# Performance work log

Hardware: AMD Instinct MI355X
Metric: run time of the kernel (lower is better)

The kernel has to match this reference:

```python
import jax, jax.numpy as jnp
import numpy as np
from jax import lax

SHIFT_SIZE = 5
PAD = SHIFT_SIZE // 2


def _chunk_shifts(C):
    # torch.chunk(x, 5, dim=1): chunk size = ceil(C/5); shift for chunk i is i - PAD
    csz = -(-C // SHIFT_SIZE)
    return jnp.arange(C) // csz - PAD  # (C,) in [-PAD, PAD]


def _shift_along_h(x, shifts):
    # x: (B,C,H,W). Equivalent of pad+chunk+roll(dim=2)+cat+narrow: per-channel
    # zero-filled shift along H (no wraparound since |shift| <= PAD).
    B, C, H, W = x.shape
    xp = jnp.pad(x, ((0, 0), (0, 0), (PAD, PAD), (0, 0)))
    c_idx = jnp.arange(C)[:, None]              # (C,1)
    h_idx = jnp.arange(H)[None, :] + PAD - shifts[:, None]  # (C,H)
    return xp[:, c_idx, h_idx, :]               # (B,C,H,W)


def _shift_along_w(x, shifts):
    return jnp.swapaxes(_shift_along_h(jnp.swapaxes(x, 2, 3), shifts), 2, 3)


def setup_inputs() -> dict:
    key = jax.random.key(0)
    ks = jax.random.split(key, 7)
    B, H, W, C, hidden = 8, 128, 128, 256, 256
    x = jax.random.normal(ks[0], (B, H * W, C), dtype=jnp.float32)
    w1 = jax.random.normal(ks[1], (hidden, C), dtype=jnp.float32) * 0.02
    b1 = jnp.zeros((hidden,), dtype=jnp.float32)
    fan_out = 3 * 3 * hidden // hidden  # groups = hidden
    dw_w = jax.random.normal(ks[2], (hidden, 1, 3, 3), dtype=jnp.float32) * np.sqrt(2.0 / fan_out)
    dw_b = jnp.zeros((hidden,), dtype=jnp.float32)
    w2 = jax.random.normal(ks[3], (C, hidden), dtype=jnp.float32) * 0.02
    b2 = jnp.zeros((C,), dtype=jnp.float32)
    return {"x": x, "H": H, "W": W, "w1": w1, "b1": b1,
            "dw_w": dw_w, "dw_b": dw_b, "w2": w2, "b2": b2}


def reference(x, H, W, w1, b1, dw_w, dw_b, w2, b2):
    B, N, C = x.shape
    shifts = _chunk_shifts(C)

    # --- shift along H, then fc1 ---
    xn = jnp.reshape(jnp.swapaxes(x, 1, 2), (B, C, H, W))
    x_s = _shift_along_h(xn, shifts)
    x_s = jnp.swapaxes(x_s.reshape(B, C, H * W), 1, 2)   # (B,N,C)
    h = x_s @ w1.T + b1                                  # (B,N,hidden)

    # --- depthwise 3x3 conv ---
    Ch = h.shape[-1]
    himg = jnp.reshape(jnp.swapaxes(h, 1, 2), (B, Ch, H, W))
    himg = lax.conv_general_dilated(
        himg, dw_w, window_strides=(1, 1), padding=((1, 1), (1, 1)),
        feature_group_count=Ch,
        dimension_numbers=("NCHW", "OIHW", "NCHW")) + dw_b[None, :, None, None]
    h = jnp.swapaxes(himg.reshape(B, Ch, H * W), 1, 2)

    h = jax.nn.gelu(h, approximate=False)

    # --- shift along W, then fc2 ---
    hn = jnp.reshape(jnp.swapaxes(h, 1, 2), (B, Ch, H, W))
    h_s = _shift_along_w(hn, _chunk_shifts(Ch))
    h_s = jnp.swapaxes(h_s.reshape(B, Ch, H * W), 1, 2)  # (B,N,hidden)
    out = h_s @ w2.T + b2                                # (B,N,C)
    return out
```

## Files before the change

### kernel.cpp

```cpp
#include <hip/hip_runtime.h>
#include <hip/hip_bf16.h>
#include <math.h>

#define Hc   128
#define Wc   128
#define Cc   256
#define Nc   (Hc * Wc)
#define Bn   8
#define Mtot (Bn * Nc)
#define CSZ  52
#define SPAD 2

typedef unsigned short ushort4v __attribute__((ext_vector_type(4)));
typedef unsigned short ushort8  __attribute__((ext_vector_type(8)));
typedef __bf16         bf16x8   __attribute__((ext_vector_type(8)));
typedef float          f32x4    __attribute__((ext_vector_type(4)));

__device__ __forceinline__ float bf2f(unsigned short u) {
    return __uint_as_float(((unsigned)u) << 16);
}
__device__ __forceinline__ unsigned short f2bf(float f) {
    unsigned u = __float_as_uint(f);
    return (unsigned short)((u + 0x7fffu + ((u >> 16) & 1u)) >> 16);
}
__device__ __forceinline__ unsigned pk2bf(float a, float b) {
    unsigned ua = __float_as_uint(a) + 0x8000u;
    unsigned ub = __float_as_uint(b) + 0x8000u;
    return __builtin_amdgcn_perm(ub, ua, 0x07060302);
}
__device__ __forceinline__ void async16(const void* g, void* l) {
    __builtin_amdgcn_global_load_lds(
        (const __attribute__((address_space(1))) unsigned*)g,
        (__attribute__((address_space(3))) unsigned*)l, 16, 0, 0);
}

__global__ __launch_bounds__(256)
void wprep_kernel(const float* __restrict__ w1, const float* __restrict__ w2,
                  const float* __restrict__ dw_w,
                  unsigned short* __restrict__ w1b, unsigned short* __restrict__ w2b,
                  float* __restrict__ dwT)
{
    const int g = blockIdx.x * 256 + threadIdx.x;
    {
        float4 a = *(const float4*)(w1 + (size_t)g * 4);
        ushort4v o = { f2bf(a.x), f2bf(a.y), f2bf(a.z), f2bf(a.w) };
        *(ushort4v*)(w1b + (size_t)g * 4) = o;
    }
    {
        float4 a = *(const float4*)(w2 + (size_t)g * 4);
        ushort4v o = { f2bf(a.x), f2bf(a.y), f2bf(a.z), f2bf(a.w) };
        *(ushort4v*)(w2b + (size_t)g * 4) = o;
    }
    if (g < 9 * Cc) dwT[(g % 9) * Cc + g / 9] = dw_w[g];
}

__global__ __launch_bounds__(256)
void shiftcvt_kernel(const float* __restrict__ x, unsigned short* __restrict__ xb)
{
    const int gid0 = blockIdx.x * 256 + threadIdx.x;
#pragma unroll
    for (int it = 0; it < 4; ++it) {
        const int gid = gid0 + it * (4096 * 256);
        const int row = gid >> 5;
        const int c   = (gid & 31) * 8;
        const int hh  = (row >> 7) & 127;
        const int s0  = c / CSZ - SPAD;
        const int s1  = (c + 4) / CSZ - SPAD;
        const int h0  = hh - s0, h1r = hh - s1;
        float4 v0 = make_float4(0.f, 0.f, 0.f, 0.f);
        float4 v1 = make_float4(0.f, 0.f, 0.f, 0.f);
        if (h0  >= 0 && h0  < Hc)
            v0 = *(const float4*)(x + ((size_t)row + (size_t)(h0 - hh) * Wc) * Cc + c);
        if (h1r >= 0 && h1r < Hc)
            v1 = *(const float4*)(x + ((size_t)row + (size_t)(h1r - hh) * Wc) * Cc + c + 4);
        uint4 o;
        o.x = pk2bf(v0.x, v0.y); o.y = pk2bf(v0.z, v0.w);
        o.z = pk2bf(v1.x, v1.y); o.w = pk2bf(v1.z, v1.w);
        *(uint4*)(xb + (size_t)row * Cc + c) = o;
    }
}

__global__ __launch_bounds__(256)
void fc1_mfma_kernel(const unsigned short* __restrict__ xb, const unsigned short* __restrict__ w1b,
                     const float* __restrict__ b1, unsigned short* __restrict__ h1)
{
    __shared__ __align__(16) unsigned char smem[34816];
    __bf16* As = (__bf16*)smem;
    __bf16* Bs = (__bf16*)(smem + 16384);
    unsigned short* Cs = (unsigned short*)smem;

    const int tid  = threadIdx.x;
    const int lane = tid & 63;
    const int wave = tid >> 6;
    const int wm = (wave >> 1) * 64, wn = (wave & 1) * 64;

    const int lid = ((blockIdx.x & 7) << 8) | (blockIdx.x >> 3);
    const int bx  = lid >> 1;
    const int j0  = (lid & 1) * 128;
    const size_t m0 = (size_t)bx * 128;
    const int idx0 = tid, idx1 = tid + 256;

    const size_t aro0 = (m0 + (idx0 >> 2)) * Cc + (idx0 & 3) * 8;
    const size_t aro1 = (m0 + (idx1 >> 2)) * Cc + (idx1 & 3) * 8;
    const size_t bro0 = (size_t)(j0 + (idx0 >> 2)) * Cc + (idx0 & 3) * 8;
    const size_t bro1 = (size_t)(j0 + (idx1 >> 2)) * Cc + (idx1 & 3) * 8;

    auto stage = [&](int buf, int t) {
        const int k0 = t * 32;
        __bf16* adst = As + buf * 4096;
        __bf16* bdst = Bs + buf * 4096;
        async16(xb  + aro0 + k0, adst + idx0 * 8);
        async16(xb  + aro1 + k0, adst + idx1 * 8);
        async16(w1b + bro0 + k0, bdst + idx0 * 8);
        async16(w1b + bro1 + k0, bdst + idx1 * 8);
    };

    f32x4 acc[4][4] = {};
    const int kq = (lane >> 4) * 8;
    const int rr = lane & 15;

    stage(0, 0);
    __syncthreads();

    int cur = 0;
    for (int t = 0; t < 8; ++t) {
        const int nxt = cur ^ 1;
        if (t < 7) stage(nxt, t + 1);
        bf16x8 a[4], b[4];
        const __bf16* ap = As + cur * 4096;
        const __bf16* bp = Bs + cur * 4096;
#pragma unroll
        for (int i = 0; i < 4; ++i) {
            a[i] = *(const bf16x8*)(ap + (wm + i * 16 + rr) * 32 + kq);
            b[i] = *(const bf16x8*)(bp + (wn + i * 16 + rr) * 32 + kq);
        }
#pragma unroll
        for (int i = 0; i < 4; ++i)
#pragma unroll
            for (int j = 0; j < 4; ++j)
                acc[i][j] = __builtin_amdgcn_mfma_f32_16x16x32_bf16(a[i], b[j], acc[i][j], 0, 0, 0);
        __syncthreads();
        cur = nxt;
    }

    const int cq = (lane >> 4) * 4;
    const int cc = lane & 15;
    float bv[4];
#pragma unroll
    for (int j = 0; j < 4; ++j) bv[j] = b1[j0 + wn + j * 16 + cc];
#pragma unroll
    for (int i = 0; i < 4; ++i)
#pragma unroll
        for (int j = 0; j < 4; ++j) {
            const int col = wn + j * 16 + cc;
#pragma unroll
            for (int rg = 0; rg < 4; ++rg)
                Cs[(wm + i * 16 + cq + rg) * 136 + col] = f2bf(acc[i][j][rg] + bv[j]);
        }
    __syncthreads();
    {
        const int row = tid >> 1, hf = tid & 1;
        const unsigned short* src = Cs + row * 136 + hf * 64;
        unsigned short* dst = h1 + (m0 + row) * Cc + j0 + hf * 64;
#pragma unroll
        for (int i = 0; i < 8; ++i)
            *(uint4*)(dst + i * 8) = *(const uint4*)(src + i * 8);
    }
}

__global__ __launch_bounds__(256)
void zero_borders_kernel(unsigned short* __restrict__ gsh)
{
    const int gid = blockIdx.x * 256 + threadIdx.x;
    const int cg  = gid & 31;
    const int rest = gid >> 5;
    const int wi = rest & 3;
    const int bh = rest >> 2;
    const int w  = (wi & 2) ? (wi + 124) : wi;
    uint4 z; z.x = z.y = z.z = z.w = 0u;
    *(uint4*)(gsh + ((size_t)bh * 128 + w) * Cc + cg * 8) = z;
}

__global__ __launch_bounds__(256)
void dwconv_gelu_scatter_kernel(const unsigned short* __restrict__ h1,
                                const float* __restrict__ dwT, const float* __restrict__ dw_b,
                                unsigned short* __restrict__ gsh)
{
    const int t   = threadIdx.x;
    const int cg  = t & 31;
    const int wq  = t >> 5;
    const int c0  = cg * 8;
    const int bh  = blockIdx.x >> 2;
    const int qtr = blockIdx.x & 3;
    const int bb  = bh >> 7, hh = bh & 127;
    const size_t rowb = (size_t)bb * Nc + (size_t)hh * Wc;
    const int wbase = qtr * 32 + wq * 4 - 1;

    float acc[4][8];
    {
        float4 a0 = *(const float4*)(dw_b + c0);
        float4 a1 = *(const float4*)(dw_b + c0 + 4);
#pragma unroll
        for (int i = 0; i < 4; ++i) {
            acc[i][0] = a0.x; acc[i][1] = a0.y; acc[i][2] = a0.z; acc[i][3] = a0.w;
            acc[i][4] = a1.x; acc[i][5] = a1.y; acc[i][6] = a1.z; acc[i][7] = a1.w;
        }
    }

#pragma unroll
    for (int dy = -1; dy <= 1; ++dy) {
        const int y = hh + dy;
        if (y < 0 || y >= Hc) continue;
        const unsigned short* rp = h1 + ((size_t)bb * Nc + (size_t)y * Wc) * Cc + c0;
        float in[6][8];
#pragma unroll
        for (int dx = 0; dx < 6; ++dx) {
            const int w = wbase + dx;
            ushort8 raw = {0, 0, 0, 0, 0, 0, 0, 0};
            if (w >= 0 && w < Wc) raw = *(const ushort8*)(rp + (size_t)w * Cc);
#pragma unroll
            for (int c = 0; c < 8; ++c) in[dx][c] = bf2f(raw[c]);
        }
        const float* wrow = dwT + (dy + 1) * 3 * Cc + c0;
        float wr[3][8];
#pragma unroll
        for (int tx = 0; tx < 3; ++tx) {
            float4 wa = *(const float4*)(wrow + tx * Cc);
            float4 wb = *(const float4*)(wrow + tx * Cc + 4);
            wr[tx][0] = wa.x; wr[tx][1] = wa.y; wr[tx][2] = wa.z; wr[tx][3] = wa.w;
            wr[tx][4] = wb.x; wr[tx][5] = wb.y; wr[tx][6] = wb.z; wr[tx][7] = wb.w;
        }
#pragma unroll
        for (int i = 0; i < 4; ++i)
#pragma unroll
            for (int tx = 0; tx < 3; ++tx)
#pragma unroll
                for (int c = 0; c < 8; ++c)
                    acc[i][c] += in[i + tx][c] * wr[tx][c];
    }

    const int s0 = c0 / CSZ - SPAD;
    const int s1 = (c0 + 4) / CSZ - SPAD;
#pragma unroll
    for (int i = 0; i < 4; ++i) {
        float g[8];
#pragma unroll
        for (int c = 0; c < 8; ++c) {
            const float v = acc[i][c];
            const float u = v * v;
            const float a = __builtin_fmaf(0.0713548162f, u, 1.5957691216f);
            const float e = __expf(v * a);
            g[c] = v * e * __builtin_amdgcn_rcpf(e + 1.0f);
        }
        uint2 lo, hi;
        lo.x = pk2bf(g[0], g[1]); lo.y = pk2bf(g[2], g[3]);
        hi.x = pk2bf(g[4], g[5]); hi.y = pk2bf(g[6], g[7]);
        const int wo = wbase + 1 + i;
        const int w0 = wo + s0, w1 = wo + s1;
        if ((unsigned)w0 < (unsigned)Wc) *(uint2*)(gsh + (rowb + w0) * Cc + c0)     = lo;
        if ((unsigned)w1 < (unsigned)Wc) *(uint2*)(gsh + (rowb + w1) * Cc + c0 + 4) = hi;
    }
}

__global__ __launch_bounds__(256)
void fc2_mfma_kernel(const unsigned short* __restrict__ A, const unsigned short* __restrict__ w2b,
                     const float* __restrict__ b2, float* __restrict__ out)
{
    __shared__ __align__(16) unsigned char smem[32768];
    __bf16* As = (__bf16*)smem;
    __bf16* Bs = (__bf16*)(smem + 16384);

    const int tid  = threadIdx.x;
    const int lane = tid & 63;
    const int wave = tid >> 6;
    const int wm = (wave >> 1) * 64, wn = (wave & 1) * 64;

    const int lid = ((blockIdx.x & 7) << 8) | (blockIdx.x >> 3);
    const size_t m0 = (size_t)(lid >> 1) * 128;
    const int j0 = (lid & 1) * 128;
    const int idx0 = tid, idx1 = tid + 256;

    const size_t aro0 = (m0 + (idx0 >> 2)) * Cc + (idx0 & 3) * 8;
    const size_t aro1 = (m0 + (idx1 >> 2)) * Cc + (idx1 & 3) * 8;
    const size_t bro0 = (size_t)(j0 + (idx0 >> 2)) * Cc + (idx0 & 3) * 8;
    const size_t bro1 = (size_t)(j0 + (idx1 >> 2)) * Cc + (idx1 & 3) * 8;

    auto stage = [&](int buf, int t) {
        const int k0 = t * 32;
        __bf16* adst = As + buf * 4096;
        __bf16* bdst = Bs + buf * 4096;
        async16(A   + aro0 + k0, adst + idx0 * 8);
        async16(A   + aro1 + k0, adst + idx1 * 8);
        async16(w2b + bro0 + k0, bdst + idx0 * 8);
        async16(w2b + bro1 + k0, bdst + idx1 * 8);
    };

    f32x4 acc[4][4] = {};
    const int kq = (lane >> 4) * 8;
    const int rr = lane & 15;

    stage(0, 0);
    __syncthreads();

    int cur = 0;
    for (int t = 0; t < 8; ++t) {
        const int nxt = cur ^ 1;
        if (t < 7) stage(nxt, t + 1);
        bf16x8 a[4], b[4];
        const __bf16* ap = As + cur * 4096;
        const __bf16* bp = Bs + cur * 4096;
#pragma unroll
        for (int i = 0; i < 4; ++i) {
            a[i] = *(const bf16x8*)(ap + (wm + i * 16 + rr) * 32 + kq);
            b[i] = *(const bf16x8*)(bp + (wn + i * 16 + rr) * 32 + kq);
        }
#pragma unroll
        for (int i = 0; i < 4; ++i)
#pragma unroll
            for (int j = 0; j < 4; ++j)
                acc[i][j] = __builtin_amdgcn_mfma_f32_16x16x32_bf16(a[i], b[j], acc[i][j], 0, 0, 0);
        __syncthreads();
        cur = nxt;
    }

    const int cq = (lane >> 4) * 4;
    const int cc = lane & 15;
    float bv[4];
#pragma unroll
    for (int j = 0; j < 4; ++j) bv[j] = b2[j0 + wn + j * 16 + cc];
#pragma unroll
    for (int i = 0; i < 4; ++i)
#pragma unroll
        for (int j = 0; j < 4; ++j) {
            const int col = j0 + wn + j * 16 + cc;
#pragma unroll
            for (int rg = 0; rg < 4; ++rg)
                out[(m0 + wm + i * 16 + cq + rg) * Cc + col] = acc[i][j][rg] + bv[j];
        }
}

extern "C" void kernel_launch(void* const* d_in, const int* in_sizes, int n_in,
                              void* d_out, int out_size, void* d_ws, size_t ws_size,
                              hipStream_t stream) {
    const float* x    = (const float*)d_in[0];
    const float* w1   = (const float*)d_in[3];
    const float* b1   = (const float*)d_in[4];
    const float* dw_w = (const float*)d_in[5];
    const float* dw_b = (const float*)d_in[6];
    const float* w2   = (const float*)d_in[7];
    const float* b2   = (const float*)d_in[8];
    float* out = (float*)d_out;

    unsigned short* h1  = (unsigned short*)d_ws;
    unsigned short* gsh = h1 + (size_t)Mtot * Cc;
    unsigned short* w1b = gsh + (size_t)Mtot * Cc;
    unsigned short* w2b = w1b + 65536;
    float*          dwT = (float*)(w2b + 65536);

    wprep_kernel<<<dim3(64), dim3(256), 0, stream>>>(w1, w2, dw_w, w1b, w2b, dwT);
    shiftcvt_kernel<<<dim3(4096), dim3(256), 0, stream>>>(x, gsh);
    fc1_mfma_kernel<<<dim3(2 * Mtot / 128), dim3(256), 0, stream>>>(gsh, w1b, b1, h1);
    zero_borders_kernel<<<dim3(512), dim3(256), 0, stream>>>(gsh);
    dwconv_gelu_scatter_kernel<<<dim3(4 * Mtot / 128), dim3(256), 0, stream>>>(h1, dwT, dw_b, gsh);
    fc2_mfma_kernel<<<dim3(2 * Mtot / 128), dim3(256), 0, stream>>>(gsh, w2b, b2, out);
}
```

Before: 354.6 us.

## Fuse depthwise conv, GELU, W-shift and fc2 into one kernel via LDS

After: 363.2 us. 2.4% more time.

```diff
diff --git a/kernel.cpp b/kernel.cpp
--- a/kernel.cpp
+++ b/kernel.cpp
@@ -169,174 +169,174 @@
 }
 
 __global__ __launch_bounds__(256)
-void zero_borders_kernel(unsigned short* __restrict__ gsh)
+void dwfc2_kernel(const unsigned short* __restrict__ h1,
+                  const float* __restrict__ dwT, const float* __restrict__ dw_b,
+                  const unsigned short* __restrict__ w2b, const float* __restrict__ b2,
+                  float* __restrict__ out)
 {
-    const int gid = blockIdx.x * 256 + threadIdx.x;
-    const int cg  = gid & 31;
-    const int rest = gid >> 5;
-    const int wi = rest & 3;
-    const int bh = rest >> 2;
-    const int w  = (wi & 2) ? (wi + 124) : wi;
-    uint4 z; z.x = z.y = z.z = z.w = 0u;
-    *(uint4*)(gsh + ((size_t)bh * 128 + w) * Cc + cg * 8) = z;
-}
-
-__global__ __launch_bounds__(256)
-void dwconv_gelu_scatter_kernel(const unsigned short* __restrict__ h1,
-                                const float* __restrict__ dwT, const float* __restrict__ dw_b,
-                                unsigned short* __restrict__ gsh)
-{
-    const int t   = threadIdx.x;
-    const int cg  = t & 31;
-    const int wq  = t >> 5;
-    const int c0  = cg * 8;
-    const int bh  = blockIdx.x >> 2;
-    const int qtr = blockIdx.x & 3;
-    const int bb  = bh >> 7, hh = bh & 127;
-    const size_t rowb = (size_t)bb * Nc + (size_t)hh * Wc;
-    const int wbase = qtr * 32 + wq * 4 - 1;
-
-    float acc[4][8];
-    {
-        float4 a0 = *(const float4*)(dw_b + c0);
-        float4 a1 = *(const float4*)(dw_b + c0 + 4);
-#pragma unroll
-        for (int i = 0; i < 4; ++i) {
-            acc[i][0] = a0.x; acc[i][1] = a0.y; acc[i][2] = a0.z; acc[i][3] = a0.w;
-            acc[i][4] = a1.x; acc[i][5] = a1.y; acc[i][6] = a1.z; acc[i][7] = a1.w;
-        }
-    }
-
-#pragma unroll
-    for (int dy = -1; dy <= 1; ++dy) {
-        const int y = hh + dy;
-        if (y < 0 || y >= Hc) continue;
-        const unsigned short* rp = h1 + ((size_t)bb * Nc + (size_t)y * Wc) * Cc + c0;
-        float in[6][8];
-#pragma unroll
-        for (int dx = 0; dx < 6; ++dx) {
-            const int w = wbase + dx;
-            ushort8 raw = {0, 0, 0, 0, 0, 0, 0, 0};
-            if (w >= 0 && w < Wc) raw = *(const ushort8*)(rp + (size_t)w * Cc);
-#pragma unroll
-            for (int c = 0; c < 8; ++c) in[dx][c] = bf2f(raw[c]);
-        }
-        const float* wrow = dwT + (dy + 1) * 3 * Cc + c0;
-        float wr[3][8];
-#pragma unroll
-        for (int tx = 0; tx < 3; ++tx) {
-            float4 wa = *(const float4*)(wrow + tx * Cc);
-            float4 wb = *(const float4*)(wrow + tx * Cc + 4);
-            wr[tx][0] = wa.x; wr[tx][1] = wa.y; wr[tx][2] = wa.z; wr[tx][3] = wa.w;
-            wr[tx][4] = wb.x; wr[tx][5] = wb.y; wr[tx][6] = wb.z; wr[tx][7] = wb.w;
-        }
-#pragma unroll
-        for (int i = 0; i < 4; ++i)
-#pragma unroll
-            for (int tx = 0; tx < 3; ++tx)
-#pragma unroll
-                for (int c = 0; c < 8; ++c)
-                    acc[i][c] += in[i + tx][c] * wr[tx][c];
-    }
-
-    const int s0 = c0 / CSZ - SPAD;
-    const int s1 = (c0 + 4) / CSZ - SPAD;
-#pragma unroll
-    for (int i = 0; i < 4; ++i) {
-        float g[8];
-#pragma unroll
-        for (int c = 0; c < 8; ++c) {
-            const float v = acc[i][c];
-            const float u = v * v;
-            const float a = __builtin_fmaf(0.0713548162f, u, 1.5957691216f);
-            const float e = __expf(v * a);
-            g[c] = v * e * __builtin_amdgcn_rcpf(e + 1.0f);
-        }
-        uint2 lo, hi;
-        lo.x = pk2bf(g[0], g[1]); lo.y = pk2bf(g[2], g[3]);
-        hi.x = pk2bf(g[4], g[5]); hi.y = pk2bf(g[6], g[7]);
-        const int wo = wbase + 1 + i;
-        const int w0 = wo + s0, w1 = wo + s1;
-        if ((unsigned)w0 < (unsigned)Wc) *(uint2*)(gsh + (rowb + w0) * Cc + c0)     = lo;
-        if ((unsigned)w1 < (unsigned)Wc) *(uint2*)(gsh + (rowb + w1) * Cc + c0 + 4) = hi;
-    }
-}
-
-__global__ __launch_bounds__(256)
-void fc2_mfma_kernel(const unsigned short* __restrict__ A, const unsigned short* __restrict__ w2b,
-                     const float* __restrict__ b2, float* __restrict__ out)
-{
-    __shared__ __align__(16) unsigned char smem[32768];
-    __bf16* As = (__bf16*)smem;
-    __bf16* Bs = (__bf16*)(smem + 16384);
+    __shared__ __align__(16) unsigned char smem[81920];
+    unsigned char* Ash = smem;
+    __bf16* Bs = (__bf16*)(smem + 65536);
 
     const int tid  = threadIdx.x;
     const int lane = tid & 63;
     const int wave = tid >> 6;
+
+    const int lid = ((blockIdx.x & 7) << 7) | (blockIdx.x >> 3);
+    const int bb = lid >> 7, hh = lid & 127;
+    const size_t m0 = (size_t)lid * 128;
+
+    {
+        uint4 z; z.x = z.y = z.z = z.w = 0u;
+        unsigned char* p = Ash + tid * 256;
+#pragma unroll
+        for (int i = 0; i < 16; ++i) *(uint4*)(p + i * 16) = z;
+    }
+    __syncthreads();
+
+    {
+        const int cg = tid & 31;
+        const int wq = tid >> 5;
+        const int c0 = cg * 8;
+        const int s0 = c0 / CSZ - SPAD;
+        const int s1 = (c0 + 4) / CSZ - SPAD;
+
+        float bias[8];
+        {
+            float4 a0 = *(const float4*)(dw_b + c0);
+            float4 a1 = *(const float4*)(dw_b + c0 + 4);
+            bias[0] = a0.x; bias[1] = a0.y; bias[2] = a0.z; bias[3] = a0.w;
+            bias[4] = a1.x; bias[5] = a1.y; bias[6] = a1.z; bias[7] = a1.w;
+        }
+        float wt[3][3][8];
+#pragma unroll
+        for (int dy = 0; dy < 3; ++dy)
+#pragma unroll
+            for (int tx = 0; tx < 3; ++tx) {
+                const float* wp = dwT + (dy * 3 + tx) * Cc + c0;
+                float4 wa = *(const float4*)(wp);
+                float4 wb = *(const float4*)(wp + 4);
+                wt[dy][tx][0] = wa.x; wt[dy][tx][1] = wa.y;
+                wt[dy][tx][2] = wa.z; wt[dy][tx][3] = wa.w;
+                wt[dy][tx][4] = wb.x; wt[dy][tx][5] = wb.y;
+                wt[dy][tx][6] = wb.z; wt[dy][tx][7] = wb.w;
+            }
+
+#pragma unroll 1
+        for (int qtr = 0; qtr < 4; ++qtr) {
+            const int wbase = qtr * 32 + wq * 4 - 1;
+            float acc[4][8];
+#pragma unroll
+            for (int i = 0; i < 4; ++i)
+#pragma unroll
+                for (int c = 0; c < 8; ++c) acc[i][c] = bias[c];
+
+#pragma unroll
+            for (int dy = -1; dy <= 1; ++dy) {
+                const int y = hh + dy;
+                if (y < 0 || y >= Hc) continue;
+                const unsigned short* rp = h1 + ((size_t)bb * Nc + (size_t)y * Wc) * Cc + c0;
+                float in[6][8];
+#pragma unroll
+                for (int dx = 0; dx < 6; ++dx) {
+                    const int w = wbase + dx;
+                    ushort8 raw = {0, 0, 0, 0, 0, 0, 0, 0};
+                    if (w >= 0 && w < Wc) raw = *(const ushort8*)(rp + (size_t)w * Cc);
+#pragma unroll
+                    for (int c = 0; c < 8; ++c) in[dx][c] = bf2f(raw[c]);
+                }
+#pragma unroll
+                for (int i = 0; i < 4; ++i)
+#pragma unroll
+                    for (int tx = 0; tx < 3; ++tx)
+#pragma unroll
+                        for (int c = 0; c < 8; ++c)
+                            acc[i][c] += in[i + tx][c] * wt[dy + 1][tx][c];
+            }
+
+#pragma unroll
+            for (int i = 0; i < 4; ++i) {
+                float g[8];
+#pragma unroll
+                for (int c = 0; c < 8; ++c) {
+                    const float v = acc[i][c];
+                    const float u = v * v;
+                    const float a = __builtin_fmaf(0.0713548162f, u, 1.5957691216f);
+                    const float e = __expf(v * a);
+                    g[c] = v * e * __builtin_amdgcn_rcpf(e + 1.0f);
+                }
+                uint2 lo, hi;
+                lo.x = pk2bf(g[0], g[1]); lo.y = pk2bf(g[2], g[3]);
+                hi.x = pk2bf(g[4], g[5]); hi.y = pk2bf(g[6], g[7]);
+                const int wo = wbase + 1 + i;
+                const int w0 = wo + s0, w1 = wo + s1;
+                if ((unsigned)w0 < (unsigned)Wc)
+                    *(uint2*)(Ash + w0 * 512 + ((c0 * 2) ^ ((w0 & 7) << 4))) = lo;
+                if ((unsigned)w1 < (unsigned)Wc)
+                    *(uint2*)(Ash + w1 * 512 + (((c0 + 4) * 2) ^ ((w1 & 7) << 4))) = hi;
+            }
+        }
+    }
+
     const int wm = (wave >> 1) * 64, wn = (wave & 1) * 64;
-
-    const int lid = ((blockIdx.x & 7) << 8) | (blockIdx.x >> 3);
-    const size_t m0 = (size_t)(lid >> 1) * 128;
-    const int j0 = (lid & 1) * 128;
-    const int idx0 = tid, idx1 = tid + 256;
-
-    const size_t aro0 = (m0 + (idx0 >> 2)) * Cc + (idx0 & 3) * 8;
-    const size_t aro1 = (m0 + (idx1 >> 2)) * Cc + (idx1 & 3) * 8;
-    const size_t bro0 = (size_t)(j0 + (idx0 >> 2)) * Cc + (idx0 & 3) * 8;
-    const size_t bro1 = (size_t)(j0 + (idx1 >> 2)) * Cc + (idx1 & 3) * 8;
-
-    auto stage = [&](int buf, int t) {
-        const int k0 = t * 32;
-        __bf16* adst = As + buf * 4096;
-        __bf16* bdst = Bs + buf * 4096;
-        async16(A   + aro0 + k0, adst + idx0 * 8);
-        async16(A   + aro1 + k0, adst + idx1 * 8);
-        async16(w2b + bro0 + k0, bdst + idx0 * 8);
-        async16(w2b + bro1 + k0, bdst + idx1 * 8);
-    };
-
-    f32x4 acc[4][4] = {};
     const int kq = (lane >> 4) * 8;
     const int rr = lane & 15;
-
-    stage(0, 0);
-    __syncthreads();
-
-    int cur = 0;
-    for (int t = 0; t < 8; ++t) {
-        const int nxt = cur ^ 1;
-        if (t < 7) stage(nxt, t + 1);
-        bf16x8 a[4], b[4];
-        const __bf16* ap = As + cur * 4096;
-        const __bf16* bp = Bs + cur * 4096;
-#pragma unroll
-        for (int i = 0; i < 4; ++i) {
-            a[i] = *(const bf16x8*)(ap + (wm + i * 16 + rr) * 32 + kq);
-            b[i] = *(const bf16x8*)(bp + (wn + i * 16 + rr) * 32 + kq);
-        }
-#pragma unroll
-        for (int i = 0; i < 4; ++i)
-#pragma unroll
-            for (int j = 0; j < 4; ++j)
-                acc[i][j] = __builtin_amdgcn_mfma_f32_16x16x32_bf16(a[i], b[j], acc[i][j], 0, 0, 0);
-        __syncthreads();
-        cur = nxt;
-    }
-
+    const int xof = (rr & 7) << 4;
+    const int idx0 = tid, idx1 = tid + 256;
     const int cq = (lane >> 4) * 4;
     const int cc = lane & 15;
-    float bv[4];
-#pragma unroll
-    for (int j = 0; j < 4; ++j) bv[j] = b2[j0 + wn + j * 16 + cc];
-#pragma unroll
-    for (int i = 0; i < 4; ++i)
-#pragma unroll
-        for (int j = 0; j < 4; ++j) {
-            const int col = j0 + wn + j * 16 + cc;
-#pragma unroll
-            for (int rg = 0; rg < 4; ++rg)
-                out[(m0 + wm + i * 16 + cq + rg) * Cc + col] = acc[i][j][rg] + bv[j];
-        }
+
+#pragma unroll 1
+    for (int pass = 0; pass < 2; ++pass) {
+        const int j0 = pass * 128;
+        const size_t bro0 = (size_t)(j0 + (idx0 >> 2)) * Cc + (idx0 & 3) * 8;
+        const size_t bro1 = (size_t)(j0 + (idx1 >> 2)) * Cc + (idx1 & 3) * 8;
+
+        auto stageB = [&](int buf, int t) {
+            const int k0 = t * 32;
+            __bf16* bdst = Bs + buf * 4096;
+            async16(w2b + bro0 + k0, bdst + idx0 * 8);
+            async16(w2b + bro1 + k0, bdst + idx1 * 8);
+        };
+
+        f32x4 acc[4][4] = {};
+        stageB(0, 0);
+        __syncthreads();
+
+        int cur = 0;
+        for (int t = 0; t < 8; ++t) {
+            const int nxt = cur ^ 1;
+            if (t < 7) stageB(nxt, t + 1);
+            const int k0 = t * 32;
+            bf16x8 a[4], b[4];
+            const __bf16* bp = Bs + cur * 4096;
+#pragma unroll
+            for (int i = 0; i < 4; ++i) {
+                a[i] = *(const bf16x8*)(Ash + (wm + i * 16 + rr) * 512 + (((k0 + kq) * 2) ^ xof));
+                b[i] = *(const bf16x8*)(bp + (wn + i * 16 + rr) * 32 + kq);
+            }
+#pragma unroll
+            for (int i = 0; i < 4; ++i)
+#pragma unroll
+                for (int j = 0; j < 4; ++j)
+                    acc[i][j] = __builtin_amdgcn_mfma_f32_16x16x32_bf16(a[i], b[j], acc[i][j], 0, 0, 0);
+            __syncthreads();
+            cur = nxt;
+        }
+
+        float bv[4];
+#pragma unroll
+        for (int j = 0; j < 4; ++j) bv[j] = b2[j0 + wn + j * 16 + cc];
+#pragma unroll
+        for (int i = 0; i < 4; ++i)
+#pragma unroll
+            for (int j = 0; j < 4; ++j) {
+                const int col = j0 + wn + j * 16 + cc;
+#pragma unroll
+                for (int rg = 0; rg < 4; ++rg)
+                    out[(m0 + wm + i * 16 + cq + rg) * Cc + col] = acc[i][j][rg] + bv[j];
+            }
+    }
 }
 
 extern "C" void kernel_launch(void* const* d_in, const int* in_sizes, int n_in,
@@ -352,15 +352,13 @@
     float* out = (float*)d_out;
 
     unsigned short* h1  = (unsigned short*)d_ws;
-    unsigned short* gsh = h1 + (size_t)Mtot * Cc;
-    unsigned short* w1b = gsh + (size_t)Mtot * Cc;
+    unsigned short* xb  = h1 + (size_t)Mtot * Cc;
+    unsigned short* w1b = xb + (size_t)Mtot * Cc;
     unsigned short* w2b = w1b + 65536;
     float*          dwT = (float*)(w2b + 65536);
 
     wprep_kernel<<<dim3(64), dim3(256), 0, stream>>>(w1, w2, dw_w, w1b, w2b, dwT);
-    shiftcvt_kernel<<<dim3(4096), dim3(256), 0, stream>>>(x, gsh);
-    fc1_mfma_kernel<<<dim3(2 * Mtot / 128), dim3(256), 0, stream>>>(gsh, w1b, b1, h1);
-    zero_borders_kernel<<<dim3(512), dim3(256), 0, stream>>>(gsh);
-    dwconv_gelu_scatter_kernel<<<dim3(4 * Mtot / 128), dim3(256), 0, stream>>>(h1, dwT, dw_b, gsh);
-    fc2_mfma_kernel<<<dim3(2 * Mtot / 128), dim3(256), 0, stream>>>(gsh, w2b, b2, out);
-}
+    shiftcvt_kernel<<<dim3(4096), dim3(256), 0, stream>>>(x, xb);
+    fc1_mfma_kernel<<<dim3(2 * Mtot / 128), dim3(256), 0, stream>>>(xb, w1b, b1, h1);
+    dwfc2_kernel<<<dim3(Mtot / 128), dim3(256), 0, stream>>>(h1, dwT, dw_b, w2b, b2, out);
+}
```

## Fuse weight prep into shift kernel and border zeroing into dwconv kernel

Applied to the files above, without the earlier changes.

Measured after the change: 353.1 us. No clear change (-0.4%).

```diff
diff --git a/kernel.cpp b/kernel.cpp
--- a/kernel.cpp
+++ b/kernel.cpp
@@ -35,29 +35,27 @@
 }
 
 __global__ __launch_bounds__(256)
-void wprep_kernel(const float* __restrict__ w1, const float* __restrict__ w2,
-                  const float* __restrict__ dw_w,
-                  unsigned short* __restrict__ w1b, unsigned short* __restrict__ w2b,
-                  float* __restrict__ dwT)
-{
-    const int g = blockIdx.x * 256 + threadIdx.x;
-    {
-        float4 a = *(const float4*)(w1 + (size_t)g * 4);
-        ushort4v o = { f2bf(a.x), f2bf(a.y), f2bf(a.z), f2bf(a.w) };
-        *(ushort4v*)(w1b + (size_t)g * 4) = o;
-    }
-    {
-        float4 a = *(const float4*)(w2 + (size_t)g * 4);
-        ushort4v o = { f2bf(a.x), f2bf(a.y), f2bf(a.z), f2bf(a.w) };
-        *(ushort4v*)(w2b + (size_t)g * 4) = o;
-    }
-    if (g < 9 * Cc) dwT[(g % 9) * Cc + g / 9] = dw_w[g];
-}
-
-__global__ __launch_bounds__(256)
-void shiftcvt_kernel(const float* __restrict__ x, unsigned short* __restrict__ xb)
+void shiftwprep_kernel(const float* __restrict__ x, unsigned short* __restrict__ xb,
+                       const float* __restrict__ w1, const float* __restrict__ w2,
+                       const float* __restrict__ dw_w,
+                       unsigned short* __restrict__ w1b, unsigned short* __restrict__ w2b,
+                       float* __restrict__ dwT)
 {
     const int gid0 = blockIdx.x * 256 + threadIdx.x;
+    if (blockIdx.x < 64) {
+        const int g = gid0;
+        {
+            float4 a = *(const float4*)(w1 + (size_t)g * 4);
+            ushort4v o = { f2bf(a.x), f2bf(a.y), f2bf(a.z), f2bf(a.w) };
+            *(ushort4v*)(w1b + (size_t)g * 4) = o;
+        }
+        {
+            float4 a = *(const float4*)(w2 + (size_t)g * 4);
+            ushort4v o = { f2bf(a.x), f2bf(a.y), f2bf(a.z), f2bf(a.w) };
+            *(ushort4v*)(w2b + (size_t)g * 4) = o;
+        }
+        if (g < 9 * Cc) dwT[(g % 9) * Cc + g / 9] = dw_w[g];
+    }
 #pragma unroll
     for (int it = 0; it < 4; ++it) {
         const int gid = gid0 + it * (4096 * 256);
@@ -169,96 +167,96 @@
 }
 
 __global__ __launch_bounds__(256)
-void zero_borders_kernel(unsigned short* __restrict__ gsh)
-{
-    const int gid = blockIdx.x * 256 + threadIdx.x;
-    const int cg  = gid & 31;
-    const int rest = gid >> 5;
-    const int wi = rest & 3;
-    const int bh = rest >> 2;
-    const int w  = (wi & 2) ? (wi + 124) : wi;
-    uint4 z; z.x = z.y = z.z = z.w = 0u;
-    *(uint4*)(gsh + ((size_t)bh * 128 + w) * Cc + cg * 8) = z;
-}
-
-__global__ __launch_bounds__(256)
 void dwconv_gelu_scatter_kernel(const unsigned short* __restrict__ h1,
                                 const float* __restrict__ dwT, const float* __restrict__ dw_b,
                                 unsigned short* __restrict__ gsh)
 {
     const int t   = threadIdx.x;
+    const int bh  = blockIdx.x;
+    const int bb  = bh >> 7, hh = bh & 127;
+    const size_t rowb = (size_t)bb * Nc + (size_t)hh * Wc;
+
+    {
+        const int wi = t >> 6;
+        const int w  = (wi & 2) ? (wi + 124) : wi;
+        const int c8 = (t & 63) * 4;
+        uint2 z; z.x = 0u; z.y = 0u;
+        *(uint2*)(gsh + (rowb + w) * Cc + c8) = z;
+    }
+    __syncthreads();
+
     const int cg  = t & 31;
     const int wq  = t >> 5;
     const int c0  = cg * 8;
-    const int bh  = blockIdx.x >> 2;
-    const int qtr = blockIdx.x & 3;
-    const int bb  = bh >> 7, hh = bh & 127;
-    const size_t rowb = (size_t)bb * Nc + (size_t)hh * Wc;
-    const int wbase = qtr * 32 + wq * 4 - 1;
-
-    float acc[4][8];
-    {
-        float4 a0 = *(const float4*)(dw_b + c0);
-        float4 a1 = *(const float4*)(dw_b + c0 + 4);
+    const int s0  = c0 / CSZ - SPAD;
+    const int s1  = (c0 + 4) / CSZ - SPAD;
+
+#pragma unroll 1
+    for (int qtr = 0; qtr < 4; ++qtr) {
+        const int wbase = qtr * 32 + wq * 4 - 1;
+
+        float acc[4][8];
+        {
+            float4 a0 = *(const float4*)(dw_b + c0);
+            float4 a1 = *(const float4*)(dw_b + c0 + 4);
+#pragma unroll
+            for (int i = 0; i < 4; ++i) {
+                acc[i][0] = a0.x; acc[i][1] = a0.y; acc[i][2] = a0.z; acc[i][3] = a0.w;
+                acc[i][4] = a1.x; acc[i][5] = a1.y; acc[i][6] = a1.z; acc[i][7] = a1.w;
+            }
+        }
+
+#pragma unroll
+        for (int dy = -1; dy <= 1; ++dy) {
+            const int y = hh + dy;
+            if (y < 0 || y >= Hc) continue;
+            const unsigned short* rp = h1 + ((size_t)bb * Nc + (size_t)y * Wc) * Cc + c0;
+            float in[6][8];
+#pragma unroll
+            for (int dx = 0; dx < 6; ++dx) {
+                const int w = wbase + dx;
+                ushort8 raw = {0, 0, 0, 0, 0, 0, 0, 0};
+                if (w >= 0 && w < Wc) raw = *(const ushort8*)(rp + (size_t)w * Cc);
+#pragma unroll
+                for (int c = 0; c < 8; ++c) in[dx][c] = bf2f(raw[c]);
+            }
+            const float* wrow = dwT + (dy + 1) * 3 * Cc + c0;
+            float wr[3][8];
+#pragma unroll
+            for (int tx = 0; tx < 3; ++tx) {
+                float4 wa = *(const float4*)(wrow + tx * Cc);
+                float4 wb = *(const float4*)(wrow + tx * Cc + 4);
+                wr[tx][0] = wa.x; wr[tx][1] = wa.y; wr[tx][2] = wa.z; wr[tx][3] = wa.w;
+                wr[tx][4] = wb.x; wr[tx][5] = wb.y; wr[tx][6] = wb.z; wr[tx][7] = wb.w;
+            }
+#pragma unroll
+            for (int i = 0; i < 4; ++i)
+#pragma unroll
+                for (int tx = 0; tx < 3; ++tx)
+#pragma unroll
+                    for (int c = 0; c < 8; ++c)
+                        acc[i][c] += in[i + tx][c] * wr[tx][c];
+        }
+
 #pragma unroll
         for (int i = 0; i < 4; ++i) {
-            acc[i][0] = a0.x; acc[i][1] = a0.y; acc[i][2] = a0.z; acc[i][3] = a0.w;
-            acc[i][4] = a1.x; acc[i][5] = a1.y; acc[i][6] = a1.z; acc[i][7] = a1.w;
-        }
-    }
-
-#pragma unroll
-    for (int dy = -1; dy <= 1; ++dy) {
-        const int y = hh + dy;
-        if (y < 0 || y >= Hc) continue;
-        const unsigned short* rp = h1 + ((size_t)bb * Nc + (size_t)y * Wc) * Cc + c0;
-        float in[6][8];
-#pragma unroll
-        for (int dx = 0; dx < 6; ++dx) {
-            const int w = wbase + dx;
-            ushort8 raw = {0, 0, 0, 0, 0, 0, 0, 0};
-            if (w >= 0 && w < Wc) raw = *(const ushort8*)(rp + (size_t)w * Cc);
-#pragma unroll
-            for (int c = 0; c < 8; ++c) in[dx][c] = bf2f(raw[c]);
-        }
-        const float* wrow = dwT + (dy + 1) * 3 * Cc + c0;
-        float wr[3][8];
-#pragma unroll
-        for (int tx = 0; tx < 3; ++tx) {
-            float4 wa = *(const float4*)(wrow + tx * Cc);
-            float4 wb = *(const float4*)(wrow + tx * Cc + 4);
-            wr[tx][0] = wa.x; wr[tx][1] = wa.y; wr[tx][2] = wa.z; wr[tx][3] = wa.w;
-            wr[tx][4] = wb.x; wr[tx][5] = wb.y; wr[tx][6] = wb.z; wr[tx][7] = wb.w;
-        }
-#pragma unroll
-        for (int i = 0; i < 4; ++i)
-#pragma unroll
-            for (int tx = 0; tx < 3; ++tx)
-#pragma unroll
-                for (int c = 0; c < 8; ++c)
-                    acc[i][c] += in[i + tx][c] * wr[tx][c];
-    }
-
-    const int s0 = c0 / CSZ - SPAD;
-    const int s1 = (c0 + 4) / CSZ - SPAD;
-#pragma unroll
-    for (int i = 0; i < 4; ++i) {
-        float g[8];
-#pragma unroll
-        for (int c = 0; c < 8; ++c) {
-            const float v = acc[i][c];
-            const float u = v * v;
-            const float a = __builtin_fmaf(0.0713548162f, u, 1.5957691216f);
-            const float e = __expf(v * a);
-            g[c] = v * e * __builtin_amdgcn_rcpf(e + 1.0f);
-        }
-        uint2 lo, hi;
-        lo.x = pk2bf(g[0], g[1]); lo.y = pk2bf(g[2], g[3]);
-        hi.x = pk2bf(g[4], g[5]); hi.y = pk2bf(g[6], g[7]);
-        const int wo = wbase + 1 + i;
-        const int w0 = wo + s0, w1 = wo + s1;
-        if ((unsigned)w0 < (unsigned)Wc) *(uint2*)(gsh + (rowb + w0) * Cc + c0)     = lo;
-        if ((unsigned)w1 < (unsigned)Wc) *(uint2*)(gsh + (rowb + w1) * Cc + c0 + 4) = hi;
+            float g[8];
+#pragma unroll
+            for (int c = 0; c < 8; ++c) {
+                const float v = acc[i][c];
+                const float u = v * v;
+                const float a = __builtin_fmaf(0.0713548162f, u, 1.5957691216f);
+                const float e = __expf(v * a);
+                g[c] = v * e * __builtin_amdgcn_rcpf(e + 1.0f);
+            }
+            uint2 lo, hi;
+            lo.x = pk2bf(g[0], g[1]); lo.y = pk2bf(g[2], g[3]);
+            hi.x = pk2bf(g[4], g[5]); hi.y = pk2bf(g[6], g[7]);
+            const int wo = wbase + 1 + i;
+            const int w0 = wo + s0, w1 = wo + s1;
+            if ((unsigned)w0 < (unsigned)Wc) *(uint2*)(gsh + (rowb + w0) * Cc + c0)     = lo;
+            if ((unsigned)w1 < (unsigned)Wc) *(uint2*)(gsh + (rowb + w1) * Cc + c0 + 4) = hi;
+        }
     }
 }
 
@@ -357,10 +355,8 @@
     unsigned short* w2b = w1b + 65536;
     float*          dwT = (float*)(w2b + 65536);
 
-    wprep_kernel<<<dim3(64), dim3(256), 0, stream>>>(w1, w2, dw_w, w1b, w2b, dwT);
-    shiftcvt_kernel<<<dim3(4096), dim3(256), 0, stream>>>(x, gsh);
+    shiftwprep_kernel<<<dim3(4096), dim3(256), 0, stream>>>(x, gsh, w1, w2, dw_w, w1b, w2b, dwT);
     fc1_mfma_kernel<<<dim3(2 * Mtot / 128), dim3(256), 0, stream>>>(gsh, w1b, b1, h1);
-    zero_borders_kernel<<<dim3(512), dim3(256), 0, stream>>>(gsh);
-    dwconv_gelu_scatter_kernel<<<dim3(4 * Mtot / 128), dim3(256), 0, stream>>>(h1, dwT, dw_b, gsh);
+    dwconv_gelu_scatter_kernel<<<dim3(Mtot / 128), dim3(256), 0, stream>>>(h1, dwT, dw_b, gsh);
     fc2_mfma_kernel<<<dim3(2 * Mtot / 128), dim3(256), 0, stream>>>(gsh, w2b, b2, out);
 }
```
